# Optimization experiments

Hardware: AMD Instinct MI355X
Metric: run time of the kernel (lower is better)

Reference implementation:

```python
import jax, jax.numpy as jnp
import numpy as np
from jax import lax

N, C, K, M = 131072, 128, 27, 65536
EPS = 1e-5


def setup_inputs() -> dict:
    key = jax.random.key(0)
    ks = jax.random.split(key, 8)
    w_scale = 1.0 / np.sqrt(K * C)  # sane fan-in init for stacked kernel weights
    return {
        "x": jax.random.normal(ks[0], (N, C), jnp.float32),
        "W1": jax.random.normal(ks[1], (K, C, C), jnp.float32) * w_scale,
        "gamma1": jnp.ones((C,), jnp.float32),
        "beta1": jnp.zeros((C,), jnp.float32),
        "W2": jax.random.normal(ks[2], (K, C, C), jnp.float32) * w_scale,
        "gamma2": jnp.ones((C,), jnp.float32),
        "beta2": jnp.zeros((C,), jnp.float32),
        "map1_in": jax.random.randint(ks[3], (K, M), 0, N, jnp.int32),
        "map1_out": jax.random.randint(ks[4], (K, M), 0, N, jnp.int32),
        "map2_in": jax.random.randint(ks[5], (K, M), 0, N, jnp.int32),
        "map2_out": jax.random.randint(ks[6], (K, M), 0, N, jnp.int32),
    }


def sparse_conv(x, W, idx_in, idx_out):
    # gather-GEMM-scatter over K kernel offsets (Minkowski kernel map)
    def body(acc, kmap):
        w, ii, io = kmap                      # [C,C], [M], [M]
        contrib = x[ii] @ w                   # gather [M,C] then GEMM
        return acc.at[io].add(contrib), None  # scatter-add
    out, _ = lax.scan(body, jnp.zeros((x.shape[0], W.shape[-1]), x.dtype),
                      (W, idx_in, idx_out))
    return out


def batch_norm(x, gamma, beta):
    m = jnp.mean(x, axis=0)
    v = jnp.var(x, axis=0)
    return (x - m) * lax.rsqrt(v + EPS) * gamma + beta


def reference(x, W1, gamma1, beta1, W2, gamma2, beta2,
              map1_in, map1_out, map2_in, map2_out):
    residual = x
    out = sparse_conv(x, W1, map1_in, map1_out)
    out = jax.nn.elu(batch_norm(out, gamma1, beta1))
    out = sparse_conv(out, W2, map2_in, map2_out)
    out = batch_norm(out, gamma2, beta2) + residual
    return jax.nn.elu(out)
```

## Files before the change

kernel.cpp:

```cpp
#include <hip/hip_runtime.h>

typedef unsigned short u16;
typedef unsigned int u32;

#define NPTS 131072
#define CD 128
#define KOFF 27
#define MMAP 65536
#define LDAB 136
#define LDC 132

__device__ __forceinline__ u16 f2bf(float f) {
  u32 u = __float_as_uint(f);
  u32 r = (u + 0x7fffu + ((u >> 16) & 1u)) >> 16;
  return (u16)r;
}

typedef __attribute__((ext_vector_type(8))) short bf16x8;
typedef __attribute__((ext_vector_type(4))) float f32x4;

__global__ __launch_bounds__(256) void k_convert_x(const float* __restrict__ x,
                                                   u16* __restrict__ xb) {
  long i = ((long)blockIdx.x * 256 + threadIdx.x) * 8;
  float4 a = *(const float4*)(x + i);
  float4 b = *(const float4*)(x + i + 4);
  uint4 v;
  v.x = f2bf(a.x) | ((u32)f2bf(a.y) << 16);
  v.y = f2bf(a.z) | ((u32)f2bf(a.w) << 16);
  v.z = f2bf(b.x) | ((u32)f2bf(b.y) << 16);
  v.w = f2bf(b.z) | ((u32)f2bf(b.w) << 16);
  *(uint4*)(xb + i) = v;
}

__global__ __launch_bounds__(256) void k_convert_w(const float* __restrict__ W,
                                                   u16* __restrict__ Wb) {
  int idx = blockIdx.x * 256 + threadIdx.x;
  if (idx >= KOFF * 2048) return;
  int k = idx >> 11;
  int rem = idx & 2047;
  int co = rem >> 4;
  int cc = rem & 15;
  const float* ws = W + (long)k * (CD * CD) + (long)(cc * 8) * CD + co;
  u16 t[8];
#pragma unroll
  for (int j = 0; j < 8; ++j) t[j] = f2bf(ws[j * CD]);
  uint4 v;
  v.x = t[0] | ((u32)t[1] << 16);
  v.y = t[2] | ((u32)t[3] << 16);
  v.z = t[4] | ((u32)t[5] << 16);
  v.w = t[6] | ((u32)t[7] << 16);
  ((uint4*)Wb)[idx] = v;
}

__global__ __launch_bounds__(256) void k_hist2(const int* __restrict__ mo,
                                               u32* __restrict__ hist, int bpp) {
  int p = blockIdx.x / bpp;
  int i = blockIdx.x * 256 + threadIdx.x;
  atomicAdd(&hist[(size_t)p * NPTS + mo[i]], 1u);
}

__global__ __launch_bounds__(256) void k_scanA2(const u32* __restrict__ hist,
                                                u32* __restrict__ offs,
                                                u32* __restrict__ bsum) {
  __shared__ u32 sh[256];
  int t = threadIdx.x, b = blockIdx.x;
  int p = b >> 9, rblk = b & 511;
  u32 v = hist[(size_t)p * NPTS + rblk * 256 + t];
  u32 run = v;
  sh[t] = run;
  __syncthreads();
  for (int d = 1; d < 256; d <<= 1) {
    u32 y = (t >= d) ? sh[t - d] : 0u;
    __syncthreads();
    run += y;
    sh[t] = run;
    __syncthreads();
  }
  offs[(size_t)p * (NPTS + 1) + rblk * 256 + t] = run - v;
  if (t == 255) bsum[b] = run;
}

__global__ __launch_bounds__(512) void k_scanB2(u32* __restrict__ bsum) {
  __shared__ u32 sh[512];
  int t = threadIdx.x;
  u32* bp = bsum + blockIdx.x * 512;
  u32 v = bp[t];
  u32 run = v;
  sh[t] = run;
  __syncthreads();
  for (int d = 1; d < 512; d <<= 1) {
    u32 y = (t >= d) ? sh[t - d] : 0u;
    __syncthreads();
    run += y;
    sh[t] = run;
    __syncthreads();
  }
  bp[t] = run - v;
}

__global__ __launch_bounds__(256) void k_scanC2(u32* __restrict__ offs,
                                                const u32* __restrict__ bsum, int kcnt) {
  int t = threadIdx.x, b = blockIdx.x;
  int p = b >> 9, rblk = b & 511;
  size_t base = (size_t)p * (NPTS + 1);
  offs[base + rblk * 256 + t] += bsum[b];
  if (rblk == 0 && t == 0) {
    int kc = KOFF - p * kcnt;
    if (kc > kcnt) kc = kcnt;
    offs[base + NPTS] = (u32)kc * MMAP;
  }
}

__global__ __launch_bounds__(256) void k_rank2(const int* __restrict__ mo,
                                               const u32* __restrict__ offs,
                                               u32* __restrict__ cur,
                                               u32* __restrict__ rank, int bpp) {
  int p = blockIdx.x / bpp;
  int i = blockIdx.x * 256 + threadIdx.x;
  int o = mo[i];
  rank[i] = offs[(size_t)p * (NPTS + 1) + o] + atomicAdd(&cur[(size_t)p * NPTS + o], 1u);
}

__global__ __launch_bounds__(256) void k_gemm3(const u16* __restrict__ src,
                                               const u16* __restrict__ Wb,
                                               const int* __restrict__ mi,
                                               const u32* __restrict__ rank,
                                               u16* __restrict__ contrib,
                                               int kbase) {
  __shared__ u16 As[64 * LDAB];
  __shared__ u16 Bs[128 * LDAB];
  __shared__ u32 sin[64];
  __shared__ u32 srow[64];
  const int t = threadIdx.x;
  const int b = blockIdx.x;
  const int klocal = b >> 10;
  const int i0 = klocal * MMAP + (b & 1023) * 64;

  if (t < 64) {
    sin[t] = (u32)mi[i0 + t];
    srow[t] = rank[i0 + t];
  }
  const uint4* wsrc = (const uint4*)(Wb + (long)(kbase + klocal) * (CD * CD));
#pragma unroll
  for (int i = 0; i < 8; ++i) {
    int q = i * 256 + t;
    int co = q >> 4, cc = q & 15;
    *(uint4*)&Bs[co * LDAB + cc * 8] = wsrc[q];
  }
  __syncthreads();
#pragma unroll
  for (int i = 0; i < 4; ++i) {
    int q = i * 256 + t;
    int r = q >> 4, cc = q & 15;
    long row = sin[r];
    *(uint4*)&As[r * LDAB + cc * 8] = ((const uint4*)(src + row * CD))[cc];
  }
  __syncthreads();

  const int wave = t >> 6, lane = t & 63;
  const int lr = lane & 15, quad = lane >> 4;
  const int wm = (wave & 1) * 32;
  const int wn = (wave >> 1) * 64;
  f32x4 acc[2][4] = {};
#pragma unroll
  for (int kk = 0; kk < 4; ++kk) {
    bf16x8 a[2], bfr[4];
#pragma unroll
    for (int mt = 0; mt < 2; ++mt)
      a[mt] = *(const bf16x8*)&As[(wm + mt * 16 + lr) * LDAB + (kk * 4 + quad) * 8];
#pragma unroll
    for (int nt = 0; nt < 4; ++nt)
      bfr[nt] = *(const bf16x8*)&Bs[(wn + nt * 16 + lr) * LDAB + (kk * 4 + quad) * 8];
#pragma unroll
    for (int mt = 0; mt < 2; ++mt)
#pragma unroll
      for (int nt = 0; nt < 4; ++nt)
        acc[mt][nt] = __builtin_amdgcn_mfma_f32_16x16x32_bf16(a[mt], bfr[nt], acc[mt][nt], 0, 0, 0);
  }

  __syncthreads();
  u16* Cs = As;
#pragma unroll
  for (int mt = 0; mt < 2; ++mt)
#pragma unroll
    for (int v = 0; v < 4; ++v) {
      int slot = wm + mt * 16 + quad * 4 + v;
#pragma unroll
      for (int nt = 0; nt < 4; ++nt)
        Cs[slot * LDC + wn + nt * 16 + lr] = f2bf(acc[mt][nt][v]);
    }
  __syncthreads();
#pragma unroll
  for (int i = 0; i < 4; ++i) {
    int q = i * 256 + t;
    int r = q >> 4, cc = q & 15;
    size_t rk = srow[r];
    *(uint4*)(contrib + rk * CD + cc * 8) = *(const uint4*)&Cs[r * LDC + cc * 8];
  }
}

__global__ __launch_bounds__(256, 8) void k_segreduce5(const u16* __restrict__ contrib,
                                                       const u32* __restrict__ offs,
                                                       float* __restrict__ acc,
                                                       float* __restrict__ stats,
                                                       int first, int last) {
  const int wave = threadIdx.x >> 6, lane = threadIdx.x & 63;
  const int W = blockIdx.x * 4 + wave;
  const int quad = lane >> 4, sub = lane & 15;
  const int r0 = W * 16;
  u32 ld_off = offs[r0 + (lane < 17 ? lane : 16)];
  float s0a = 0.f, s1a = 0.f, q0a = 0.f, q1a = 0.f;
#pragma unroll 2
  for (int b = 0; b < 16; ++b) {
    const int row = r0 + b;
    const u32 e0 = __shfl(ld_off, b);
    const u32 e1 = __shfl(ld_off, b + 1);
    const int len = (int)(e1 - e0);
    float v[8];
#pragma unroll
    for (int j = 0; j < 8; ++j) v[j] = 0.f;
    const u32* cp = (const u32*)(contrib + (size_t)e0 * CD) + sub * 4;
    for (int i = quad; i < len; i += 4) {
      uint4 d = *(const uint4*)(cp + (size_t)i * 64);
      v[0] += __uint_as_float(d.x << 16);
      v[1] += __uint_as_float(d.x & 0xffff0000u);
      v[2] += __uint_as_float(d.y << 16);
      v[3] += __uint_as_float(d.y & 0xffff0000u);
      v[4] += __uint_as_float(d.z << 16);
      v[5] += __uint_as_float(d.z & 0xffff0000u);
      v[6] += __uint_as_float(d.w << 16);
      v[7] += __uint_as_float(d.w & 0xffff0000u);
    }
#pragma unroll
    for (int j = 0; j < 8; ++j) {
      v[j] += __shfl_xor(v[j], 16);
      v[j] += __shfl_xor(v[j], 32);
    }
    float2* ap = (float2*)(acc + (size_t)row * CD) + (sub * 4 + quad);
    float c0 = v[2 * quad], c1 = v[2 * quad + 1];
    if (!first) {
      float2 pv = *ap;
      c0 += pv.x;
      c1 += pv.y;
    }
    *ap = make_float2(c0, c1);
    if (last) {
      s0a += c0;
      q0a += c0 * c0;
      s1a += c1;
      q1a += c1 * c1;
    }
  }
  if (last) {
    __shared__ float sh[256][4];
    sh[threadIdx.x][0] = s0a;
    sh[threadIdx.x][1] = s1a;
    sh[threadIdx.x][2] = q0a;
    sh[threadIdx.x][3] = q1a;
    __syncthreads();
    if (threadIdx.x < 64) {
      int l = threadIdx.x;
      int c = (l & 15) * 8 + (l >> 4) * 2;
      float S0 = sh[l][0] + sh[64 + l][0] + sh[128 + l][0] + sh[192 + l][0];
      float S1 = sh[l][1] + sh[64 + l][1] + sh[128 + l][1] + sh[192 + l][1];
      float Q0 = sh[l][2] + sh[64 + l][2] + sh[128 + l][2] + sh[192 + l][2];
      float Q1 = sh[l][3] + sh[64 + l][3] + sh[128 + l][3] + sh[192 + l][3];
      atomicAdd(&stats[c], S0);
      atomicAdd(&stats[c + 1], S1);
      atomicAdd(&stats[128 + c], Q0);
      atomicAdd(&stats[128 + c + 1], Q1);
    }
  }
}

__global__ void k_finalize(const float* __restrict__ stats, const float* __restrict__ gamma,
                           const float* __restrict__ beta, float* __restrict__ scsh) {
  int c = threadIdx.x;
  float mean = stats[c] * (1.f / NPTS);
  float var = stats[128 + c] * (1.f / NPTS) - mean * mean;
  float sc = rsqrtf(var + 1e-5f) * gamma[c];
  scsh[c] = sc;
  scsh[128 + c] = beta[c] - mean * sc;
}

__device__ __forceinline__ float elu(float v) { return v > 0.f ? v : expf(v) - 1.f; }

__global__ __launch_bounds__(256) void k_apply_mid(const float* __restrict__ acc,
                                                   const float* __restrict__ scsh,
                                                   u16* __restrict__ y) {
  long i = ((long)blockIdx.x * 256 + threadIdx.x) * 4;
  int c = (int)(i & 127);
  float4 a = *(const float4*)(acc + i);
  float r0 = elu(a.x * scsh[c] + scsh[128 + c]);
  float r1 = elu(a.y * scsh[c + 1] + scsh[129 + c]);
  float r2 = elu(a.z * scsh[c + 2] + scsh[130 + c]);
  float r3 = elu(a.w * scsh[c + 3] + scsh[131 + c]);
  uint2 v;
  v.x = f2bf(r0) | ((u32)f2bf(r1) << 16);
  v.y = f2bf(r2) | ((u32)f2bf(r3) << 16);
  *(uint2*)(y + i) = v;
}

__global__ __launch_bounds__(256) void k_apply_final(const float* __restrict__ acc,
                                                     const float* __restrict__ scsh,
                                                     const float* __restrict__ x,
                                                     float* __restrict__ out) {
  long i = ((long)blockIdx.x * 256 + threadIdx.x) * 4;
  int c = (int)(i & 127);
  float4 a = *(const float4*)(acc + i);
  float4 rx = *(const float4*)(x + i);
  float4 o;
  o.x = elu(a.x * scsh[c] + scsh[128 + c] + rx.x);
  o.y = elu(a.y * scsh[c + 1] + scsh[129 + c] + rx.y);
  o.z = elu(a.z * scsh[c + 2] + scsh[130 + c] + rx.z);
  o.w = elu(a.w * scsh[c + 3] + scsh[131 + c] + rx.w);
  *(float4*)(out + i) = o;
}

extern "C" void kernel_launch(void* const* d_in, const int* in_sizes, int n_in,
                              void* d_out, int out_size, void* d_ws, size_t ws_size,
                              hipStream_t stream) {
  const float* x = (const float*)d_in[0];
  const float* W1 = (const float*)d_in[1];
  const float* g1 = (const float*)d_in[2];
  const float* b1 = (const float*)d_in[3];
  const float* W2 = (const float*)d_in[4];
  const float* g2 = (const float*)d_in[5];
  const float* b2 = (const float*)d_in[6];
  const int* m1i = (const int*)d_in[7];
  const int* m1o = (const int*)d_in[8];
  const int* m2i = (const int*)d_in[9];
  const int* m2o = (const int*)d_in[10];
  float* out = (float*)d_out;

  char* base = (char*)d_ws;
  size_t off = 0;
  auto alloc = [&](size_t bytes) -> void* {
    void* r = base + off;
    off = (off + bytes + 255) & ~(size_t)255;
    return r;
  };
  u16* xb = (u16*)alloc((size_t)NPTS * CD * 2);
  u16* Wb1 = (u16*)alloc((size_t)KOFF * CD * CD * 2);
  u16* Wb2 = (u16*)alloc((size_t)KOFF * CD * CD * 2);
  float* acc = (float*)alloc((size_t)NPTS * CD * 4);
  float* stats = (float*)alloc(256 * 4);
  float* scsh = (float*)alloc(256 * 4);

  int kcnt = 1, P = KOFF;
  for (int kc = KOFF; kc >= 1; --kc) {
    int Pp = (KOFF + kc - 1) / kc;
    size_t need = off + 2 * (size_t)Pp * NPTS * 4 + 512
                  + (size_t)Pp * (NPTS + 1) * 4 + 256
                  + (size_t)Pp * 512 * 4 + 256
                  + (size_t)KOFF * MMAP * 4 + 256
                  + (size_t)kc * MMAP * CD * 2 + 4096;
    if (need <= ws_size) {
      kcnt = kc;
      P = Pp;
      break;
    }
  }
  u32* hist = (u32*)alloc((size_t)P * NPTS * 4);
  u32* cur = (u32*)alloc((size_t)P * NPTS * 4);
  u32* offs = (u32*)alloc((size_t)P * (NPTS + 1) * 4);
  u32* bsum = (u32*)alloc((size_t)P * 512 * 4);
  u32* rank = (u32*)alloc((size_t)KOFF * MMAP * 4);
  u16* contrib = (u16*)alloc((size_t)kcnt * MMAP * CD * 2);

  k_convert_x<<<(NPTS * CD) / 2048, 256, 0, stream>>>(x, xb);
  k_convert_w<<<(KOFF * 2048 + 255) / 256, 256, 0, stream>>>(W1, Wb1);
  k_convert_w<<<(KOFF * 2048 + 255) / 256, 256, 0, stream>>>(W2, Wb2);

  const int nb = (KOFF * MMAP) / 256;
  const int bpp = kcnt * (MMAP / 256);

  auto run_conv = [&](const u16* srcm, const u16* Wbm, const int* mi, const int* mo) {
    hipMemsetAsync(stats, 0, 1024, stream);
    hipMemsetAsync(hist, 0, 2 * (size_t)P * NPTS * 4, stream);
    k_hist2<<<nb, 256, 0, stream>>>(mo, hist, bpp);
    k_scanA2<<<512 * P, 256, 0, stream>>>(hist, offs, bsum);
    k_scanB2<<<P, 512, 0, stream>>>(bsum);
    k_scanC2<<<512 * P, 256, 0, stream>>>(offs, bsum, kcnt);
    k_rank2<<<nb, 256, 0, stream>>>(mo, offs, cur, rank, bpp);
    for (int p = 0; p < P; ++p) {
      int kc = (KOFF - p * kcnt < kcnt) ? KOFF - p * kcnt : kcnt;
      k_gemm3<<<kc * 1024, 256, 0, stream>>>(srcm, Wbm, mi + (long)p * kcnt * MMAP,
                                             rank + (long)p * kcnt * MMAP, contrib, p * kcnt);
      k_segreduce5<<<2048, 256, 0, stream>>>(contrib, offs + (size_t)p * (NPTS + 1), acc, stats,
                                             p == 0 ? 1 : 0, p == P - 1 ? 1 : 0);
    }
  };

  run_conv(xb, Wb1, m1i, m1o);
  k_finalize<<<1, 128, 0, stream>>>(stats, g1, b1, scsh);
  k_apply_mid<<<(NPTS * CD) / 1024, 256, 0, stream>>>(acc, scsh, xb);

  run_conv(xb, Wb2, m2i, m2o);
  k_finalize<<<1, 128, 0, stream>>>(stats, g2, b2, scsh);
  k_apply_final<<<(NPTS * CD) / 1024, 256, 0, stream>>>(acc, scsh, x, out);
}
```

Baseline: 1.335 ms.

## Replace row-segmented reduce with entry-parallel run-length reduce plus separate stats pass

The reduction over sorted contributions now parallelises over sorted entries rather than output rows. Each wave loads 64 contiguous contrib rows, sums runs that share an output index, and writes them to acc, using float atomics only for runs that cross a 16-entry chunk boundary. To support this, k_rank2 writes the sorted output-row keys, and acc is zeroed up front and again in k_apply_mid. BN statistics move to a separate k_stats pass over acc. The change targets the load imbalance and serial per-row loops of variable-length segments, at the cost of an extra full read of acc, atomics, and more register pressure from 16 uint4 loads per lane.

```diff
diff --git a/kernel.cpp b/kernel.cpp
--- a/kernel.cpp
+++ b/kernel.cpp
@@ -114,11 +114,14 @@
 __global__ __launch_bounds__(256) void k_rank2(const int* __restrict__ mo,
                                                const u32* __restrict__ offs,
                                                u32* __restrict__ cur,
-                                               u32* __restrict__ rank, int bpp) {
+                                               u32* __restrict__ rank,
+                                               u32* __restrict__ srt, int bpp) {
   int p = blockIdx.x / bpp;
   int i = blockIdx.x * 256 + threadIdx.x;
   int o = mo[i];
-  rank[i] = offs[(size_t)p * (NPTS + 1) + o] + atomicAdd(&cur[(size_t)p * NPTS + o], 1u);
+  u32 r = offs[(size_t)p * (NPTS + 1) + o] + atomicAdd(&cur[(size_t)p * NPTS + o], 1u);
+  rank[i] = r;
+  srt[(size_t)p * bpp * 256 + r] = (u32)o;
 }
 
 __global__ __launch_bounds__(256) void k_gemm3(const u16* __restrict__ src,
@@ -199,76 +202,109 @@
   }
 }
 
-__global__ __launch_bounds__(256, 8) void k_segreduce5(const u16* __restrict__ contrib,
-                                                       const u32* __restrict__ offs,
+__global__ __launch_bounds__(256, 4) void k_segreduce6(const u16* __restrict__ contrib,
+                                                       const u32* __restrict__ srt,
                                                        float* __restrict__ acc,
-                                                       float* __restrict__ stats,
-                                                       int first, int last) {
+                                                       u32 total) {
   const int wave = threadIdx.x >> 6, lane = threadIdx.x & 63;
-  const int W = blockIdx.x * 4 + wave;
-  const int quad = lane >> 4, sub = lane & 15;
-  const int r0 = W * 16;
-  u32 ld_off = offs[r0 + (lane < 17 ? lane : 16)];
-  float s0a = 0.f, s1a = 0.f, q0a = 0.f, q1a = 0.f;
-#pragma unroll 2
-  for (int b = 0; b < 16; ++b) {
-    const int row = r0 + b;
-    const u32 e0 = __shfl(ld_off, b);
-    const u32 e1 = __shfl(ld_off, b + 1);
-    const int len = (int)(e1 - e0);
-    float v[8];
-#pragma unroll
-    for (int j = 0; j < 8; ++j) v[j] = 0.f;
-    const u32* cp = (const u32*)(contrib + (size_t)e0 * CD) + sub * 4;
-    for (int i = quad; i < len; i += 4) {
-      uint4 d = *(const uint4*)(cp + (size_t)i * 64);
-      v[0] += __uint_as_float(d.x << 16);
-      v[1] += __uint_as_float(d.x & 0xffff0000u);
-      v[2] += __uint_as_float(d.y << 16);
-      v[3] += __uint_as_float(d.y & 0xffff0000u);
-      v[4] += __uint_as_float(d.z << 16);
-      v[5] += __uint_as_float(d.z & 0xffff0000u);
-      v[6] += __uint_as_float(d.w << 16);
-      v[7] += __uint_as_float(d.w & 0xffff0000u);
-    }
-#pragma unroll
-    for (int j = 0; j < 8; ++j) {
-      v[j] += __shfl_xor(v[j], 16);
-      v[j] += __shfl_xor(v[j], 32);
-    }
-    float2* ap = (float2*)(acc + (size_t)row * CD) + (sub * 4 + quad);
-    float c0 = v[2 * quad], c1 = v[2 * quad + 1];
-    if (!first) {
-      float2 pv = *ap;
-      c0 += pv.x;
-      c1 += pv.y;
-    }
-    *ap = make_float2(c0, c1);
-    if (last) {
-      s0a += c0;
-      q0a += c0 * c0;
-      s1a += c1;
-      q1a += c1 * c1;
-    }
-  }
-  if (last) {
-    __shared__ float sh[256][4];
-    sh[threadIdx.x][0] = s0a;
-    sh[threadIdx.x][1] = s1a;
-    sh[threadIdx.x][2] = q0a;
-    sh[threadIdx.x][3] = q1a;
-    __syncthreads();
-    if (threadIdx.x < 64) {
-      int l = threadIdx.x;
-      int c = (l & 15) * 8 + (l >> 4) * 2;
-      float S0 = sh[l][0] + sh[64 + l][0] + sh[128 + l][0] + sh[192 + l][0];
-      float S1 = sh[l][1] + sh[64 + l][1] + sh[128 + l][1] + sh[192 + l][1];
-      float Q0 = sh[l][2] + sh[64 + l][2] + sh[128 + l][2] + sh[192 + l][2];
-      float Q1 = sh[l][3] + sh[64 + l][3] + sh[128 + l][3] + sh[192 + l][3];
-      atomicAdd(&stats[c], S0);
-      atomicAdd(&stats[c + 1], S1);
-      atomicAdd(&stats[128 + c], Q0);
-      atomicAdd(&stats[128 + c + 1], Q1);
+  const u32 e_base = (blockIdx.x * 4 + wave) * 64;
+  const int q = lane >> 4, sub = lane & 15;
+
+  u32 kk = srt[e_base + lane];
+  u32 prevk = (q == 0) ? ((e_base == 0) ? 0xFFFFFFFFu : srt[e_base - 1])
+                       : __shfl(kk, 16 * q - 1);
+  u32 nextk = (q == 3) ? ((e_base + 64 >= total) ? 0xFFFFFFFFu : srt[e_base + 64])
+                       : __shfl(kk, 16 * q + 16);
+
+  uint4 d[16];
+#pragma unroll
+  for (int i = 0; i < 16; ++i)
+    d[i] = *(const uint4*)(contrib + (size_t)(e_base + 16 * q + i) * CD + sub * 8);
+
+  float run[8];
+  auto set8 = [&](uint4 dd) {
+    run[0] = __uint_as_float(dd.x << 16);
+    run[1] = __uint_as_float(dd.x & 0xffff0000u);
+    run[2] = __uint_as_float(dd.y << 16);
+    run[3] = __uint_as_float(dd.y & 0xffff0000u);
+    run[4] = __uint_as_float(dd.z << 16);
+    run[5] = __uint_as_float(dd.z & 0xffff0000u);
+    run[6] = __uint_as_float(dd.w << 16);
+    run[7] = __uint_as_float(dd.w & 0xffff0000u);
+  };
+  auto add8 = [&](uint4 dd) {
+    run[0] += __uint_as_float(dd.x << 16);
+    run[1] += __uint_as_float(dd.x & 0xffff0000u);
+    run[2] += __uint_as_float(dd.y << 16);
+    run[3] += __uint_as_float(dd.y & 0xffff0000u);
+    run[4] += __uint_as_float(dd.z << 16);
+    run[5] += __uint_as_float(dd.z & 0xffff0000u);
+    run[6] += __uint_as_float(dd.w << 16);
+    run[7] += __uint_as_float(dd.w & 0xffff0000u);
+  };
+  auto emit = [&](u32 row, bool at) {
+    float* ap = acc + (size_t)row * CD + sub * 8;
+    if (at) {
+#pragma unroll
+      for (int j = 0; j < 8; ++j) atomicAdd(ap + j, run[j]);
+    } else {
+      float4 p0 = *(float4*)ap;
+      float4 p1 = *(float4*)(ap + 4);
+      p0.x += run[0]; p0.y += run[1]; p0.z += run[2]; p0.w += run[3];
+      p1.x += run[4]; p1.y += run[5]; p1.z += run[6]; p1.w += run[7];
+      *(float4*)ap = p0;
+      *(float4*)(ap + 4) = p1;
+    }
+  };
+
+  u32 curk = __shfl(kk, 16 * q);
+  set8(d[0]);
+  bool firstRun = true;
+#pragma unroll
+  for (int i = 1; i < 16; ++i) {
+    u32 ki = __shfl(kk, 16 * q + i);
+    if (ki == curk) {
+      add8(d[i]);
+    } else {
+      emit(curk, firstRun && (curk == prevk));
+      curk = ki;
+      set8(d[i]);
+      firstRun = false;
+    }
+  }
+  emit(curk, (curk == nextk) || (firstRun && (curk == prevk)));
+}
+
+__global__ __launch_bounds__(256) void k_stats(const float* __restrict__ acc,
+                                               float* __restrict__ stats) {
+  const int t = threadIdx.x;
+  const long total = (long)NPTS * CD / 4;
+  const long stride = (long)gridDim.x * 256;
+  long idx = (long)blockIdx.x * 256 + t;
+  float s0 = 0.f, s1 = 0.f, s2 = 0.f, s3 = 0.f;
+  float q0 = 0.f, q1 = 0.f, q2 = 0.f, q3 = 0.f;
+  for (long i = idx; i < total; i += stride) {
+    float4 a = *(const float4*)(acc + i * 4);
+    s0 += a.x; q0 += a.x * a.x;
+    s1 += a.y; q1 += a.y * a.y;
+    s2 += a.z; q2 += a.z * a.z;
+    s3 += a.w; q3 += a.w * a.w;
+  }
+  __shared__ float sh[2048];
+  sh[t * 8 + 0] = s0; sh[t * 8 + 1] = s1; sh[t * 8 + 2] = s2; sh[t * 8 + 3] = s3;
+  sh[t * 8 + 4] = q0; sh[t * 8 + 5] = q1; sh[t * 8 + 6] = q2; sh[t * 8 + 7] = q3;
+  __syncthreads();
+  if (t < 32) {
+#pragma unroll
+    for (int j = 0; j < 4; ++j) {
+      float a = 0.f, qq = 0.f;
+#pragma unroll
+      for (int g = 0; g < 8; ++g) {
+        a += sh[(t + g * 32) * 8 + j];
+        qq += sh[(t + g * 32) * 8 + 4 + j];
+      }
+      atomicAdd(&stats[t * 4 + j], a);
+      atomicAdd(&stats[128 + t * 4 + j], qq);
     }
   }
 }
@@ -285,7 +321,7 @@
 
 __device__ __forceinline__ float elu(float v) { return v > 0.f ? v : expf(v) - 1.f; }
 
-__global__ __launch_bounds__(256) void k_apply_mid(const float* __restrict__ acc,
+__global__ __launch_bounds__(256) void k_apply_mid(float* __restrict__ acc,
                                                    const float* __restrict__ scsh,
                                                    u16* __restrict__ y) {
   long i = ((long)blockIdx.x * 256 + threadIdx.x) * 4;
@@ -299,6 +335,7 @@
   v.x = f2bf(r0) | ((u32)f2bf(r1) << 16);
   v.y = f2bf(r2) | ((u32)f2bf(r3) << 16);
   *(uint2*)(y + i) = v;
+  *(float4*)(acc + i) = make_float4(0.f, 0.f, 0.f, 0.f);
 }
 
 __global__ __launch_bounds__(256) void k_apply_final(const float* __restrict__ acc,
@@ -354,6 +391,7 @@
                   + (size_t)Pp * (NPTS + 1) * 4 + 256
                   + (size_t)Pp * 512 * 4 + 256
                   + (size_t)KOFF * MMAP * 4 + 256
+                  + (size_t)Pp * kc * MMAP * 4 + 256
                   + (size_t)kc * MMAP * CD * 2 + 4096;
     if (need <= ws_size) {
       kcnt = kc;
@@ -366,8 +404,10 @@
   u32* offs = (u32*)alloc((size_t)P * (NPTS + 1) * 4);
   u32* bsum = (u32*)alloc((size_t)P * 512 * 4);
   u32* rank = (u32*)alloc((size_t)KOFF * MMAP * 4);
+  u32* srt = (u32*)alloc((size_t)P * kcnt * MMAP * 4);
   u16* contrib = (u16*)alloc((size_t)kcnt * MMAP * CD * 2);
 
+  hipMemsetAsync(acc, 0, (size_t)NPTS * CD * 4, stream);
   k_convert_x<<<(NPTS * CD) / 2048, 256, 0, stream>>>(x, xb);
   k_convert_w<<<(KOFF * 2048 + 255) / 256, 256, 0, stream>>>(W1, Wb1);
   k_convert_w<<<(KOFF * 2048 + 255) / 256, 256, 0, stream>>>(W2, Wb2);
@@ -382,14 +422,15 @@
     k_scanA2<<<512 * P, 256, 0, stream>>>(hist, offs, bsum);
     k_scanB2<<<P, 512, 0, stream>>>(bsum);
     k_scanC2<<<512 * P, 256, 0, stream>>>(offs, bsum, kcnt);
-    k_rank2<<<nb, 256, 0, stream>>>(mo, offs, cur, rank, bpp);
+    k_rank2<<<nb, 256, 0, stream>>>(mo, offs, cur, rank, srt, bpp);
     for (int p = 0; p < P; ++p) {
       int kc = (KOFF - p * kcnt < kcnt) ? KOFF - p * kcnt : kcnt;
       k_gemm3<<<kc * 1024, 256, 0, stream>>>(srcm, Wbm, mi + (long)p * kcnt * MMAP,
                                              rank + (long)p * kcnt * MMAP, contrib, p * kcnt);
-      k_segreduce5<<<2048, 256, 0, stream>>>(contrib, offs + (size_t)p * (NPTS + 1), acc, stats,
-                                             p == 0 ? 1 : 0, p == P - 1 ? 1 : 0);
-    }
+      k_segreduce6<<<kc * 256, 256, 0, stream>>>(contrib, srt + (size_t)p * kcnt * MMAP, acc,
+                                                 (u32)kc * MMAP);
+    }
+    k_stats<<<2048, 256, 0, stream>>>(acc, stats);
   };
 
   run_conv(xb, Wb1, m1i, m1o);
```

Result: slower. 2.380 ms (+78.3%).
